# Optimization experiments

Measured on AMD Instinct MI355X. Metric: run time of the kernel, lower is better.

## Reference

```python
import jax, jax.numpy as jnp
import numpy as np

NUM_CLASSES = 80
STRIDES = (8, 16, 32)


def _decode(p, stride):
    # p: [B, 5+C, H, W] raw head -> [B, HW, 5+C] decoded (xy in px, wh=exp*stride)
    B, C, H, W = p.shape
    ys, xs = jnp.meshgrid(jnp.arange(H), jnp.arange(W), indexing='ij')
    grid = jnp.stack([xs, ys], -1).reshape(H * W, 2).astype(p.dtype)
    out = p.reshape(B, C, H * W).transpose(0, 2, 1)
    xy = (out[..., :2] + grid) * stride
    wh = jnp.exp(out[..., 2:4]) * stride
    out = jnp.concatenate([xy, wh, out[..., 4:]], -1)
    es = jnp.full((H * W,), float(stride), p.dtype)
    return out, grid[:, 0], grid[:, 1], es


def _pairwise_iou(gt, pr):
    # gt [G,4] cxcywh, pr [A,4] -> [G,A]
    gt_tl = gt[:, None, :2] - gt[:, None, 2:] * 0.5
    gt_br = gt[:, None, :2] + gt[:, None, 2:] * 0.5
    pr_tl = pr[None, :, :2] - pr[None, :, 2:] * 0.5
    pr_br = pr[None, :, :2] + pr[None, :, 2:] * 0.5
    tl = jnp.maximum(gt_tl, pr_tl)
    br = jnp.minimum(gt_br, pr_br)
    en = jnp.all(tl < br, -1).astype(gt.dtype)
    inter = jnp.prod(br - tl, -1) * en
    a_gt = jnp.prod(gt[:, 2:], -1)[:, None]
    a_pr = jnp.prod(pr[:, 2:], -1)[None, :]
    return inter / (a_gt + a_pr - inter + 1e-16)


def _assign(gt_boxes, gt_cls, bbox, clsp, objp, xg, yg, es):
    # SimOTA assignment for one image (all fixed-shape; non-candidate anchors
    # are masked out via huge cost instead of boolean gather).
    G = gt_boxes.shape[0]
    xc = (xg + 0.5) * es  # [A] anchor centers
    yc = (yg + 0.5) * es
    gl = gt_boxes[:, 0:1] - 0.5 * gt_boxes[:, 2:3]
    gr = gt_boxes[:, 0:1] + 0.5 * gt_boxes[:, 2:3]
    gt_ = gt_boxes[:, 1:2] - 0.5 * gt_boxes[:, 3:4]
    gb = gt_boxes[:, 1:2] + 0.5 * gt_boxes[:, 3:4]
    in_box = (xc[None] > gl) & (xc[None] < gr) & (yc[None] > gt_) & (yc[None] < gb)  # [G,A]
    r = 2.5 * es[None]
    in_ctr = ((xc[None] > gt_boxes[:, 0:1] - r) & (xc[None] < gt_boxes[:, 0:1] + r)
              & (yc[None] > gt_boxes[:, 1:2] - r) & (yc[None] < gt_boxes[:, 1:2] + r))
    fg_cand = jnp.any(in_box, 0) | jnp.any(in_ctr, 0)  # [A]
    in_both = in_box & in_ctr  # [G,A]

    ious = _pairwise_iou(gt_boxes, bbox)  # [G,A]
    ious_m = jnp.where(fg_cand[None, :], ious, 0.0)
    iou_cost = -jnp.log(ious_m + 1e-8)

    # pairwise cls BCE cost: bce(sqrt(sigmoid(cls)*sigmoid(obj)), onehot(gt)).sum(-1)
    p = jnp.sqrt(jax.nn.sigmoid(clsp) * jax.nn.sigmoid(objp[:, None]))  # [A,C]
    lp = jnp.maximum(jnp.log(p), -100.0)
    l1p = jnp.maximum(jnp.log1p(-p), -100.0)
    t = jax.nn.one_hot(gt_cls, NUM_CLASSES, dtype=p.dtype)  # [G,C]
    cls_cost = -(jnp.einsum('ac,gc->ga', lp - l1p, t) + jnp.sum(l1p, -1)[None, :])

    cost = (cls_cost + 3.0 * iou_cost
            + 1e5 * (~in_both).astype(p.dtype)
            + 1e9 * (~fg_cand)[None, :].astype(p.dtype))

    # dynamic-k: k_g = clamp(sum(top10 ious), min=1)
    topk_ious, _ = jax.lax.top_k(ious_m, 10)
    dyn_k = jnp.clip(topk_ious.sum(-1).astype(jnp.int32), 1, None)  # [G]
    rank = jnp.argsort(jnp.argsort(cost, axis=1), axis=1)  # rank of each anchor per gt
    matching = (rank < dyn_k[:, None]) & fg_cand[None, :]  # [G,A]
    # resolve anchors matched to multiple gts: keep min-cost gt
    multi = matching.sum(0) > 1
    best = jnp.argmin(cost, 0)
    matching = jnp.where(multi[None, :], jnp.arange(G)[:, None] == best[None, :], matching)

    fg = jnp.any(matching, 0)  # [A]
    matched_gt = jnp.argmax(matching, 0)  # [A]
    pred_iou = jnp.sum(matching * ious, 0)  # [A]
    matched_cls = gt_cls[matched_gt]
    return fg, matched_gt, pred_iou, matched_cls


def _giou_loss(b, g):
    tl = jnp.maximum(b[..., :2] - b[..., 2:] * 0.5, g[..., :2] - g[..., 2:] * 0.5)
    br = jnp.minimum(b[..., :2] + b[..., 2:] * 0.5, g[..., :2] + g[..., 2:] * 0.5)
    area_b = jnp.prod(b[..., 2:], -1)
    area_g = jnp.prod(g[..., 2:], -1)
    en = jnp.all(tl < br, -1).astype(b.dtype)
    inter = jnp.prod(br - tl, -1) * en
    union = area_b + area_g - inter
    iou = inter / (union + 1e-16)
    ctl = jnp.minimum(b[..., :2] - b[..., 2:] * 0.5, g[..., :2] - g[..., 2:] * 0.5)
    cbr = jnp.maximum(b[..., :2] + b[..., 2:] * 0.5, g[..., :2] + g[..., 2:] * 0.5)
    area_c = jnp.maximum(jnp.prod(cbr - ctl, -1), 1e-16)
    giou = iou - (area_c - union) / area_c
    return 1.0 - jnp.clip(giou, -1.0, 1.0)


def _bce_logits(x, t):
    return jnp.maximum(x, 0.0) - x * t + jnp.log1p(jnp.exp(-jnp.abs(x)))


def _forward(p8, p16, p32, labels):
    outs, xo, yo, eo = [], [], [], []
    for p, s in zip((p8, p16, p32), STRIDES):
        o, x, y, e = _decode(p, s)
        outs.append(o); xo.append(x); yo.append(y); eo.append(e)
    outputs = jnp.concatenate(outs, 1)  # [B, A, 5+C]
    xg = jnp.concatenate(xo); yg = jnp.concatenate(yo); es = jnp.concatenate(eo)

    bbox = outputs[..., :4]
    obj = outputs[..., 4]
    cls = outputs[..., 5:]
    gt_boxes = labels[..., :4]
    gt_cls = labels[..., 4].astype(jnp.int32)

    # assignment runs under no_grad in torch
    det = jax.lax.stop_gradient(outputs)
    fg, matched_gt, pred_iou, matched_cls = jax.vmap(
        lambda gb, gc, o: _assign(gb, gc, o[..., :4], o[..., 5:], o[..., 4], xg, yg, es)
    )(gt_boxes, gt_cls, det)

    fgf = fg.astype(outputs.dtype)  # [B,A]
    reg_t = jnp.take_along_axis(gt_boxes, matched_gt[..., None], axis=1)  # [B,A,4]
    cls_t = (jax.nn.one_hot(matched_cls, NUM_CLASSES, dtype=outputs.dtype)
             * pred_iou[..., None] * fgf[..., None])

    loss_iou = jnp.sum(_giou_loss(bbox, reg_t) * fgf)
    loss_obj = jnp.sum(_bce_logits(obj, fgf))
    loss_cls = jnp.sum(_bce_logits(cls, cls_t) * fgf[..., None])
    num_fg = jnp.maximum(jnp.sum(fgf), 1.0)
    return (5.0 * loss_iou + loss_obj + loss_cls) / num_fg


def setup_inputs() -> dict:
    key = jax.random.key(0)
    k1, k2, k3, k4, k5, k6 = jax.random.split(key, 6)
    B, NGT = 32, 20
    p8 = jax.random.normal(k1, (B, 5 + NUM_CLASSES, 80, 80), dtype=jnp.float32)
    p16 = jax.random.normal(k2, (B, 5 + NUM_CLASSES, 40, 40), dtype=jnp.float32)
    p32 = jax.random.normal(k3, (B, 5 + NUM_CLASSES, 20, 20), dtype=jnp.float32)
    cxy = jax.random.uniform(k4, (B, NGT, 2), dtype=jnp.float32, minval=32.0, maxval=608.0)
    wh = jax.random.uniform(k5, (B, NGT, 2), dtype=jnp.float32, minval=16.0, maxval=128.0)
    cls = jax.random.randint(k6, (B, NGT, 1), 0, NUM_CLASSES).astype(jnp.float32)
    labels = jnp.concatenate([cxy, wh, cls], -1)
    return {"p8": p8, "p16": p16, "p32": p32, "labels": labels}


def reference(p8, p16, p32, labels):
    return _forward(p8, p16, p32, labels)
```

## Files before the change

kernel.cpp:

```cpp
#include <hip/hip_runtime.h>
#include <cstdint>
#include <cstddef>

#define NA 8400
#define NAP 8448
#define NB 32
#define NG 20
#define NCL 80
#define NBLK 33
#define KC_BLKS 12

__device__ __forceinline__ float frcp(float x) { return __builtin_amdgcn_rcpf(x); }
__device__ __forceinline__ float bce0(float x) {
  return fmaxf(x, 0.0f) + __logf(1.0f + __expf(-fabsf(x)));
}

__device__ __forceinline__ void anchor_info(int a, const float* p8, const float* p16,
                                            const float* p32, int b, const float*& base,
                                            int& hw, int& HW, int& xg, int& yg, float& fs) {
  if (a < 6400)      { hw = a;        HW = 6400; xg = hw % 80; yg = hw / 80; fs = 8.f;
                       base = p8  + (size_t)b * 85 * 6400; }
  else if (a < 8000) { hw = a - 6400; HW = 1600; xg = hw % 40; yg = hw / 40; fs = 16.f;
                       base = p16 + (size_t)b * 85 * 1600; }
  else               { hw = a - 8000; HW = 400;  xg = hw % 20; yg = hw / 20; fs = 32.f;
                       base = p32 + (size_t)b * 85 * 400; }
}

__device__ __forceinline__ float iou_raw(float gx, float gy, float gw, float gh, float4 p) {
  float gtlx = gx - gw * 0.5f, gtly = gy - gh * 0.5f;
  float gbrx = gx + gw * 0.5f, gbry = gy + gh * 0.5f;
  float ptlx = p.x - p.z * 0.5f, ptly = p.y - p.w * 0.5f;
  float pbrx = p.x + p.z * 0.5f, pbry = p.y + p.w * 0.5f;
  float tlx = fmaxf(gtlx, ptlx), tly = fmaxf(gtly, ptly);
  float brx = fminf(gbrx, pbrx), bry = fminf(gbry, pbry);
  float inter = ((tlx < brx) && (tly < bry)) ? (brx - tlx) * (bry - tly) : 0.0f;
  float ag = gw * gh, ap = p.z * p.w;
  return inter * frcp(ag + ap - inter + 1e-16f);
}

__device__ __forceinline__ float giou_loss(float4 bb, float gx, float gy, float gw, float gh) {
  float btlx = bb.x - bb.z * 0.5f, btly = bb.y - bb.w * 0.5f;
  float bbrx = bb.x + bb.z * 0.5f, bbry = bb.y + bb.w * 0.5f;
  float gtlx = gx - gw * 0.5f, gtly = gy - gh * 0.5f;
  float gbrx = gx + gw * 0.5f, gbry = gy + gh * 0.5f;
  float tlx = fmaxf(btlx, gtlx), tly = fmaxf(btly, gtly);
  float brx = fminf(bbrx, gbrx), bry = fminf(bbry, gbry);
  float area_b = bb.z * bb.w, area_g = gw * gh;
  float inter = ((tlx < brx) && (tly < bry)) ? (brx - tlx) * (bry - tly) : 0.0f;
  float uni = area_b + area_g - inter;
  float iou = inter / (uni + 1e-16f);
  float ctlx = fminf(btlx, gtlx), ctly = fminf(btly, gtly);
  float cbrx = fmaxf(bbrx, gbrx), cbry = fmaxf(bbry, gbry);
  float area_c = fmaxf((cbrx - ctlx) * (cbry - ctly), 1e-16f);
  float giou = iou - (area_c - uni) / area_c;
  giou = fminf(fmaxf(giou, -1.0f), 1.0f);
  return 1.0f - giou;
}

__device__ __forceinline__ void block_argmin(float& v, int& i, volatile float* s_v,
                                             volatile int* s_i, int tid) {
#pragma unroll
  for (int off = 32; off; off >>= 1) {
    float ov = __shfl_down(v, off, 64);
    int   oi = __shfl_down(i, off, 64);
    if (ov < v || (ov == v && oi < i)) { v = ov; i = oi; }
  }
  if ((tid & 63) == 0) { s_v[tid >> 6] = v; s_i[tid >> 6] = i; }
  __syncthreads();
  v = s_v[0]; i = s_i[0];
#pragma unroll
  for (int w = 1; w < 4; ++w) {
    float ov = s_v[w]; int oi = s_i[w];
    if (ov < v || (ov == v && oi < i)) { v = ov; i = oi; }
  }
}

__global__ __launch_bounds__(256) void k1(const float* __restrict__ p8,
                                          const float* __restrict__ p16,
                                          const float* __restrict__ p32,
                                          const float* __restrict__ labels,
                                          int* __restrict__ n_fg_cnt,
                                          int* __restrict__ fg_list,
                                          unsigned int* __restrict__ am_c,
                                          float4* __restrict__ bbox_c,
                                          float* __restrict__ lso_c,
                                          unsigned int* __restrict__ match_c,
                                          float* __restrict__ blk_obj) {
  __shared__ float s_gt[NG * 4];
  __shared__ unsigned int s_wcnt[4];
  __shared__ float s_part[4];
  __shared__ unsigned int s_base;
  int blk = blockIdx.x, b = blockIdx.y, tid = threadIdx.x, lane = tid & 63, wid = tid >> 6;

  if (tid < NG) {
    s_gt[tid * 4 + 0] = labels[((size_t)b * NG + tid) * 5 + 0];
    s_gt[tid * 4 + 1] = labels[((size_t)b * NG + tid) * 5 + 1];
    s_gt[tid * 4 + 2] = labels[((size_t)b * NG + tid) * 5 + 2];
    s_gt[tid * 4 + 3] = labels[((size_t)b * NG + tid) * 5 + 3];
  }
  __syncthreads();

  int a = blk * 256 + tid;
  match_c[(size_t)b * NAP + a] = 0u;

  bool fg = false;
  unsigned int msk = 0u;
  float bce_obj = 0.0f, obj = 0.0f;
  const float* base = nullptr; int hw = 0, HW = 0, xg = 0, yg = 0; float fs = 8.f;
  if (a < NA) {
    anchor_info(a, p8, p16, p32, b, base, hw, HW, xg, yg, fs);
    obj = base[4 * HW + hw];
    bce_obj = bce0(obj);
    float xc = ((float)xg + 0.5f) * fs;
    float yc = ((float)yg + 0.5f) * fs;
    float r = 2.5f * fs;
#pragma unroll
    for (int g = 0; g < NG; ++g) {
      float gx = s_gt[g * 4 + 0], gy = s_gt[g * 4 + 1];
      float gw = s_gt[g * 4 + 2], gh = s_gt[g * 4 + 3];
      bool inb = (xc > gx - 0.5f * gw) && (xc < gx + 0.5f * gw) &&
                 (yc > gy - 0.5f * gh) && (yc < gy + 0.5f * gh);
      bool inc = (xc > gx - r) && (xc < gx + r) && (yc > gy - r) && (yc < gy + r);
      fg = fg || inb || inc;
      if (inb && inc) msk |= (1u << g);
    }
  }

  unsigned long long bm = __ballot(fg);
#pragma unroll
  for (int off = 32; off; off >>= 1) bce_obj += __shfl_down(bce_obj, off, 64);
  if (lane == 0) { s_wcnt[wid] = (unsigned int)__popcll(bm); s_part[wid] = bce_obj; }
  __syncthreads();
  if (tid == 0) {
    unsigned int cnt = s_wcnt[0] + s_wcnt[1] + s_wcnt[2] + s_wcnt[3];
    s_base = cnt ? (unsigned int)atomicAdd(&n_fg_cnt[b], (int)cnt) : 0u;
    blk_obj[b * NBLK + blk] = s_part[0] + s_part[1] + s_part[2] + s_part[3];
  }
  __syncthreads();

  if (!fg) return;
  unsigned int pos = s_base;
  for (int w = 0; w < wid; ++w) pos += s_wcnt[w];
  pos += (unsigned int)__popcll(bm & ((1ull << lane) - 1ull));
  size_t bo = (size_t)b * NAP;
  int ci = (int)pos;
  fg_list[bo + ci] = a;
  am_c[bo + ci] = msk;

  float v0 = base[hw];
  float v1 = base[HW + hw];
  float v2 = base[2 * HW + hw];
  float v3 = base[3 * HW + hw];
  bbox_c[bo + ci] = make_float4((v0 + (float)xg) * fs, (v1 + (float)yg) * fs,
                                __expf(v2) * fs, __expf(v3) * fs);
  float uo = __logf(1.0f + __expf(-fabsf(obj)));
  lso_c[bo + ci] = fminf(obj, 0.0f) - uo;
}

__global__ __launch_bounds__(256) void k2(const float* __restrict__ p8,
                                          const float* __restrict__ p16,
                                          const float* __restrict__ p32,
                                          const int* __restrict__ fg_list,
                                          const int* __restrict__ n_fg,
                                          const float* __restrict__ lso_c,
                                          float* __restrict__ sl_c,
                                          float* __restrict__ sb_c) {
  __shared__ float s_sl[8][33];
  __shared__ float s_sb[8][33];
  int b = blockIdx.y, tid = threadIdx.x;
  int part = tid >> 5, cl = tid & 31;
  int n = n_fg[b];
  size_t bo = (size_t)b * NAP;

  for (int base_ci = blockIdx.x * 32; base_ci < n; base_ci += gridDim.x * 32) {
    int ci = base_ci + cl;
    bool act = ci < n;
    float sl = 0.0f, sb = 0.0f;
    if (act) {
      int a = fg_list[bo + ci];
      float lso = lso_c[bo + ci];
      const float* base; int hw, HW, xg, yg; float fs;
      anchor_info(a, p8, p16, p32, b, base, hw, HW, xg, yg, fs);
      const float* cb = base + (size_t)(5 + part * 10) * HW + hw;
      float xs[10];
#pragma unroll
      for (int j = 0; j < 5; ++j) xs[j] = cb[j * HW];
#pragma unroll
      for (int j = 5; j < 10; ++j) xs[j] = cb[j * HW];
#pragma unroll
      for (int j = 0; j < 10; ++j) {
        float x = xs[j];
        float u = __logf(1.0f + __expf(-fabsf(x)));
        sb += fmaxf(x, 0.0f) + u;
        float lsx = fminf(x, 0.0f) - u;
        float lpr = 0.5f * (lsx + lso);
        float p   = __expf(lpr);
        sl += fmaxf(__logf(1.0f - p), -100.0f);
      }
    }
    s_sl[part][cl] = sl;
    s_sb[part][cl] = sb;
    __syncthreads();
    if (tid < 32 && base_ci + tid < n) {
      float tsl = 0.0f, tsb = 0.0f;
#pragma unroll
      for (int q = 0; q < 8; ++q) { tsl += s_sl[q][tid]; tsb += s_sb[q][tid]; }
      sl_c[bo + base_ci + tid] = tsl;
      sb_c[bo + base_ci + tid] = tsb;
    }
    __syncthreads();
  }
}

__global__ __launch_bounds__(256) void k3(const float* __restrict__ p8,
                                          const float* __restrict__ p16,
                                          const float* __restrict__ p32,
                                          const float* __restrict__ labels,
                                          const int* __restrict__ fg_list,
                                          const int* __restrict__ n_fg,
                                          const float* __restrict__ lso_c,
                                          const float* __restrict__ sl_c,
                                          const float4* __restrict__ bbox_c,
                                          const unsigned int* __restrict__ am_c,
                                          float* __restrict__ cost_tbl,
                                          float* __restrict__ iou_tbl) {
  int g = blockIdx.y, b = blockIdx.z, tid = threadIdx.x;
  int n = n_fg[b];
  size_t bo = (size_t)b * NAP;
  float gx = labels[((size_t)b * NG + g) * 5 + 0];
  float gy = labels[((size_t)b * NG + g) * 5 + 1];
  float gw = labels[((size_t)b * NG + g) * 5 + 2];
  float gh = labels[((size_t)b * NG + g) * 5 + 3];
  int   cg = (int)labels[((size_t)b * NG + g) * 5 + 4];
  size_t row = ((size_t)b * NG + g) * NAP;

  for (int ci = blockIdx.x * 256 + tid; ci < n; ci += gridDim.x * 256) {
    int a = fg_list[bo + ci];
    unsigned int am = am_c[bo + ci];
    float lso = lso_c[bo + ci];
    float sl  = sl_c[bo + ci];
    float4 pb = bbox_c[bo + ci];
    const float* base; int hw, HW, xg, yg; float fs;
    anchor_info(a, p8, p16, p32, b, base, hw, HW, xg, yg, fs);
    float x = base[(size_t)(5 + cg) * HW + hw];

    float u = __logf(1.0f + __expf(-fabsf(x)));
    float lsx = fminf(x, 0.0f) - u;
    float lpr = 0.5f * (lsx + lso);
    float p   = __expf(lpr);
    float l1p = fmaxf(__logf(1.0f - p), -100.0f);
    float wv  = fmaxf(lpr, -100.0f) - l1p;
    float iou = iou_raw(gx, gy, gw, gh, pb);
    float cst = -(wv + sl) - 3.0f * __logf(iou + 1e-8f);
    if (!((am >> g) & 1u)) cst += 100000.0f;
    cost_tbl[row + ci] = cst;
    iou_tbl[row + ci]  = iou;
  }
}

__global__ __launch_bounds__(256) void kB(const float* __restrict__ cost_tbl,
                                          const float* __restrict__ iou_tbl,
                                          const int* __restrict__ n_fg,
                                          unsigned int* __restrict__ match_c) {
  __shared__ float s_cost[NAP];
  __shared__ float s_wt[4 * 10];
  __shared__ float s_v[4];
  __shared__ int   s_i[4];
  __shared__ int   s_k;

  int g = blockIdx.x, b = blockIdx.y, tid = threadIdx.x;
  int lane = tid & 63, wid = tid >> 6;
  int n = n_fg[b];
  size_t bo = (size_t)b * NAP;
  const float* __restrict__ cg = cost_tbl + ((size_t)b * NG + g) * NAP;
  const float* __restrict__ ig = iou_tbl  + ((size_t)b * NG + g) * NAP;

  float t10[10];
#pragma unroll
  for (int j = 0; j < 10; ++j) t10[j] = 0.0f;

  for (int ci = tid; ci < n; ci += 256) {
    float iou = ig[ci];
    float cst = cg[ci];
    if (iou > t10[9]) {
      t10[9] = iou;
#pragma unroll
      for (int q = 9; q > 0; --q) {
        if (t10[q] > t10[q - 1]) { float t = t10[q]; t10[q] = t10[q - 1]; t10[q - 1] = t; }
        else break;
      }
    }
    s_cost[ci] = cst;
  }

  for (int r = 0; r < 10; ++r) {
    float v = t10[0];
    float bv = v;
#pragma unroll
    for (int off = 32; off; off >>= 1) bv = fmaxf(bv, __shfl_down(bv, off, 64));
    bv = __shfl(bv, 0, 64);
    unsigned long long won = __ballot(v == bv);
    if (lane == __ffsll(won) - 1) {
#pragma unroll
      for (int q = 0; q < 9; ++q) t10[q] = t10[q + 1];
      t10[9] = -1.0f;
    }
    if (lane == 0) s_wt[wid * 10 + r] = bv;
  }
  __syncthreads();

  if (tid == 0) {
    int p0 = 0, p1 = 0, p2 = 0, p3 = 0;
    float s = 0.0f;
    for (int r = 0; r < 10; ++r) {
      float v0 = (p0 < 10) ? s_wt[p0]      : -2.0f;
      float v1 = (p1 < 10) ? s_wt[10 + p1] : -2.0f;
      float v2 = (p2 < 10) ? s_wt[20 + p2] : -2.0f;
      float v3 = (p3 < 10) ? s_wt[30 + p3] : -2.0f;
      float m = fmaxf(fmaxf(v0, v1), fmaxf(v2, v3));
      s += m;
      if (m == v0) ++p0; else if (m == v1) ++p1; else if (m == v2) ++p2; else ++p3;
    }
    int k = (int)s;
    if (k < 1) k = 1;
    s_k = k;
  }
  __syncthreads();
  int k = s_k;

  for (int it = 0; it < k; ++it) {
    float bv = 3.4e38f; int bi = NAP;
    for (int ci = tid; ci < n; ci += 256) {
      float v = s_cost[ci];
      if (v < bv || (v == bv && ci < bi)) { bv = v; bi = ci; }
    }
    block_argmin(bv, bi, s_v, s_i, tid);
    if (bv >= 1e8f) break;
    if (tid == 0) {
      atomicOr(&match_c[bo + bi], 1u << g);
      s_cost[bi] = 3.4e38f;
    }
    __syncthreads();
  }
}

__global__ __launch_bounds__(256) void kCD(const float* __restrict__ p8,
                                           const float* __restrict__ p16,
                                           const float* __restrict__ p32,
                                           const float* __restrict__ labels,
                                           const float4* __restrict__ bbox_c,
                                           const float* __restrict__ sb_c,
                                           const float* __restrict__ cost_tbl,
                                           const float* __restrict__ iou_tbl,
                                           const int* __restrict__ fg_list,
                                           const int* __restrict__ n_fg,
                                           const unsigned int* __restrict__ match_c,
                                           const float* __restrict__ blk_obj,
                                           float* __restrict__ accum,
                                           int* __restrict__ done_cnt,
                                           float* __restrict__ out) {
  __shared__ float s_gt[NG * 5];
  __shared__ float s_red[16];
  __shared__ int s_last;
  int b = blockIdx.y, tid = threadIdx.x;
  if (tid < NG * 5) s_gt[tid] = labels[(size_t)b * NG * 5 + tid];
  __syncthreads();

  int n = n_fg[b];
  size_t bo = (size_t)b * NAP;
  float li = 0.0f, oe = 0.0f, lc = 0.0f, nf = 0.0f;

  for (int ci = blockIdx.x * 256 + tid; ci < n; ci += KC_BLKS * 256) {
    unsigned int m = match_c[bo + ci];
    if (m == 0u) continue;
    int mg;
    if (m & (m - 1)) {
      float bestc = 3.4e38f; mg = 0;
#pragma unroll 4
      for (int g = 0; g < NG; ++g) {
        float cst = cost_tbl[((size_t)b * NG + g) * NAP + ci];
        if (cst < bestc) { bestc = cst; mg = g; }
      }
    } else {
      mg = __ffs(m) - 1;
    }
    int a = fg_list[bo + ci];
    const float* base; int hw, HW, xg, yg; float fs;
    anchor_info(a, p8, p16, p32, b, base, hw, HW, xg, yg, fs);
    float4 pb = bbox_c[bo + ci];
    float gx = s_gt[mg * 5], gy = s_gt[mg * 5 + 1];
    float gw = s_gt[mg * 5 + 2], gh = s_gt[mg * 5 + 3];
    int cg = (int)s_gt[mg * 5 + 4];
    float piou = iou_tbl[((size_t)b * NG + mg) * NAP + ci];
    li += giou_loss(pb, gx, gy, gw, gh);
    float xcls = base[(size_t)(5 + cg) * HW + hw];
    lc += sb_c[bo + ci] - xcls * piou;
    oe += base[4 * HW + hw];
    nf += 1.0f;
  }

  float vals[4] = {li, oe, lc, nf};
#pragma unroll
  for (int q = 0; q < 4; ++q) {
#pragma unroll
    for (int off = 32; off; off >>= 1) vals[q] += __shfl_down(vals[q], off, 64);
  }
  if ((tid & 63) == 0) {
    int wid = tid >> 6;
    s_red[wid * 4 + 0] = vals[0];
    s_red[wid * 4 + 1] = vals[1];
    s_red[wid * 4 + 2] = vals[2];
    s_red[wid * 4 + 3] = vals[3];
  }
  __syncthreads();
  if (tid < 4) {
    const int slot[4] = {0, 2, 3, 4};
    float s = s_red[tid] + s_red[4 + tid] + s_red[8 + tid] + s_red[12 + tid];
    atomicAdd(&accum[slot[tid]], s);
  }

  if (tid == 0) {
    __threadfence();
    int old = atomicAdd(done_cnt, 1);
    s_last = (old == KC_BLKS * NB - 1) ? 1 : 0;
  }
  __syncthreads();
  if (s_last) {
    float s = 0.0f;
    for (int i = tid; i < NB * NBLK; i += 256) s += blk_obj[i];
#pragma unroll
    for (int off = 32; off; off >>= 1) s += __shfl_down(s, off, 64);
    if ((tid & 63) == 0) s_red[tid >> 6] = s;
    __syncthreads();
    if (tid == 0) {
      float obj_base = s_red[0] + s_red[1] + s_red[2] + s_red[3];
      float loss_iou = atomicAdd(&accum[0], 0.0f);
      float oex      = atomicAdd(&accum[2], 0.0f);
      float loss_cls = atomicAdd(&accum[3], 0.0f);
      float num_fg   = atomicAdd(&accum[4], 0.0f);
      float loss_obj = obj_base - oex;
      out[0] = (5.0f * loss_iou + loss_obj + loss_cls) / fmaxf(num_fg, 1.0f);
    }
  }
}

extern "C" void kernel_launch(void* const* d_in, const int* in_sizes, int n_in,
                              void* d_out, int out_size, void* d_ws, size_t ws_size,
                              hipStream_t stream) {
  const float* p8     = (const float*)d_in[0];
  const float* p16    = (const float*)d_in[1];
  const float* p32    = (const float*)d_in[2];
  const float* labels = (const float*)d_in[3];
  float* out = (float*)d_out;

  const size_t BAP = (size_t)NB * NAP;
  char* w = (char*)d_ws;
  float4*       bbox_c   = (float4*)w;
  float*        cost_tbl = (float*)(w + BAP * 16);
  float*        iou_tbl  = cost_tbl + (size_t)NB * NG * NAP;
  char*         w2       = (char*)(iou_tbl + (size_t)NB * NG * NAP);
  int*          fg_list  = (int*)(w2);
  unsigned int* match_c  = (unsigned int*)(w2 + BAP * 4);
  float*        sb_c     = (float*)(w2 + BAP * 8);
  float*        sl_c     = (float*)(w2 + BAP * 12);
  float*        lso_c    = (float*)(w2 + BAP * 16);
  unsigned int* am_c     = (unsigned int*)(w2 + BAP * 20);
  char*         w3       = w2 + BAP * 24;
  int*          n_fg     = (int*)w3;
  float*        accum    = (float*)(w3 + 128);
  int*          done_cnt = (int*)(w3 + 160);
  float*        blk_obj  = (float*)(w3 + 256);

  hipMemsetAsync(w3, 0, 256, stream);

  k1<<<dim3(NBLK, NB), dim3(256), 0, stream>>>(p8, p16, p32, labels, n_fg, fg_list, am_c,
                                               bbox_c, lso_c, match_c, blk_obj);
  k2<<<dim3(24, NB), dim3(256), 0, stream>>>(p8, p16, p32, fg_list, n_fg, lso_c, sl_c, sb_c);
  k3<<<dim3(12, NG, NB), dim3(256), 0, stream>>>(p8, p16, p32, labels, fg_list, n_fg, lso_c,
                                                 sl_c, bbox_c, am_c, cost_tbl, iou_tbl);
  kB<<<dim3(NG, NB), dim3(256), 0, stream>>>(cost_tbl, iou_tbl, n_fg, match_c);
  kCD<<<dim3(KC_BLKS, NB), dim3(256), 0, stream>>>(p8, p16, p32, labels, bbox_c, sb_c,
                                                   cost_tbl, iou_tbl, fg_list, n_fg,
                                                   match_c, blk_obj, accum, done_cnt, out);
}
```

Before: 173.4 us.

## Fuse cls-cost and per-GT cost kernels, and fold loss reduction into matching kernel

Merges the per-anchor class-sum kernel with the per-GT cost/IoU table kernel, so the summed log term stays in shared memory instead of a global sl_c buffer and the anchor metadata is loaded once per anchor. Also merges the top-k matching kernel with the final loss kernel: the last GT block per image, found with an atomic counter, computes that image's loss terms, and the last image finalizes the output. This removes two launches and one intermediate buffer. In exchange, the final per-image loss runs in a single block and the cost kernel uses fewer blocks.

```diff
diff --git a/kernel.cpp b/kernel.cpp
--- a/kernel.cpp
+++ b/kernel.cpp
@@ -8,7 +8,6 @@
 #define NG 20
 #define NCL 80
 #define NBLK 33
-#define KC_BLKS 12
 
 __device__ __forceinline__ float frcp(float x) { return __builtin_amdgcn_rcpf(x); }
 __device__ __forceinline__ float bce0(float x) {
@@ -157,36 +156,51 @@
   lso_c[bo + ci] = fminf(obj, 0.0f) - uo;
 }
 
-__global__ __launch_bounds__(256) void k2(const float* __restrict__ p8,
-                                          const float* __restrict__ p16,
-                                          const float* __restrict__ p32,
-                                          const int* __restrict__ fg_list,
-                                          const int* __restrict__ n_fg,
-                                          const float* __restrict__ lso_c,
-                                          float* __restrict__ sl_c,
-                                          float* __restrict__ sb_c) {
+__global__ __launch_bounds__(256) void k23(const float* __restrict__ p8,
+                                           const float* __restrict__ p16,
+                                           const float* __restrict__ p32,
+                                           const float* __restrict__ labels,
+                                           const int* __restrict__ fg_list,
+                                           const int* __restrict__ n_fg,
+                                           const float* __restrict__ lso_c,
+                                           const unsigned int* __restrict__ am_c,
+                                           const float4* __restrict__ bbox_c,
+                                           float* __restrict__ sb_c,
+                                           float* __restrict__ cost_tbl,
+                                           float* __restrict__ iou_tbl) {
+  __shared__ float s_gt[NG * 4];
+  __shared__ int   s_gcls[NG];
   __shared__ float s_sl[8][33];
   __shared__ float s_sb[8][33];
+  __shared__ float s_slr[32];
   int b = blockIdx.y, tid = threadIdx.x;
   int part = tid >> 5, cl = tid & 31;
+
+  if (tid < NG) {
+    s_gt[tid * 4 + 0] = labels[((size_t)b * NG + tid) * 5 + 0];
+    s_gt[tid * 4 + 1] = labels[((size_t)b * NG + tid) * 5 + 1];
+    s_gt[tid * 4 + 2] = labels[((size_t)b * NG + tid) * 5 + 2];
+    s_gt[tid * 4 + 3] = labels[((size_t)b * NG + tid) * 5 + 3];
+    s_gcls[tid] = (int)labels[((size_t)b * NG + tid) * 5 + 4];
+  }
+  __syncthreads();
+
   int n = n_fg[b];
   size_t bo = (size_t)b * NAP;
 
   for (int base_ci = blockIdx.x * 32; base_ci < n; base_ci += gridDim.x * 32) {
     int ci = base_ci + cl;
     bool act = ci < n;
-    float sl = 0.0f, sb = 0.0f;
+    const float* base = nullptr; int hw = 0, HW = 0, xg, yg; float fs;
+    float lso = 0.0f, sl = 0.0f, sb = 0.0f;
     if (act) {
       int a = fg_list[bo + ci];
-      float lso = lso_c[bo + ci];
-      const float* base; int hw, HW, xg, yg; float fs;
+      lso = lso_c[bo + ci];
       anchor_info(a, p8, p16, p32, b, base, hw, HW, xg, yg, fs);
       const float* cb = base + (size_t)(5 + part * 10) * HW + hw;
       float xs[10];
 #pragma unroll
-      for (int j = 0; j < 5; ++j) xs[j] = cb[j * HW];
-#pragma unroll
-      for (int j = 5; j < 10; ++j) xs[j] = cb[j * HW];
+      for (int j = 0; j < 10; ++j) xs[j] = cb[(size_t)j * HW];
 #pragma unroll
       for (int j = 0; j < 10; ++j) {
         float x = xs[j];
@@ -201,72 +215,68 @@
     s_sl[part][cl] = sl;
     s_sb[part][cl] = sb;
     __syncthreads();
-    if (tid < 32 && base_ci + tid < n) {
+    if (tid < 32) {
       float tsl = 0.0f, tsb = 0.0f;
 #pragma unroll
       for (int q = 0; q < 8; ++q) { tsl += s_sl[q][tid]; tsb += s_sb[q][tid]; }
-      sl_c[bo + base_ci + tid] = tsl;
-      sb_c[bo + base_ci + tid] = tsb;
+      s_slr[tid] = tsl;
+      if (base_ci + tid < n) sb_c[bo + base_ci + tid] = tsb;
     }
     __syncthreads();
-  }
-}
-
-__global__ __launch_bounds__(256) void k3(const float* __restrict__ p8,
-                                          const float* __restrict__ p16,
-                                          const float* __restrict__ p32,
-                                          const float* __restrict__ labels,
-                                          const int* __restrict__ fg_list,
-                                          const int* __restrict__ n_fg,
-                                          const float* __restrict__ lso_c,
-                                          const float* __restrict__ sl_c,
-                                          const float4* __restrict__ bbox_c,
-                                          const unsigned int* __restrict__ am_c,
-                                          float* __restrict__ cost_tbl,
-                                          float* __restrict__ iou_tbl) {
-  int g = blockIdx.y, b = blockIdx.z, tid = threadIdx.x;
-  int n = n_fg[b];
-  size_t bo = (size_t)b * NAP;
-  float gx = labels[((size_t)b * NG + g) * 5 + 0];
-  float gy = labels[((size_t)b * NG + g) * 5 + 1];
-  float gw = labels[((size_t)b * NG + g) * 5 + 2];
-  float gh = labels[((size_t)b * NG + g) * 5 + 3];
-  int   cg = (int)labels[((size_t)b * NG + g) * 5 + 4];
-  size_t row = ((size_t)b * NG + g) * NAP;
-
-  for (int ci = blockIdx.x * 256 + tid; ci < n; ci += gridDim.x * 256) {
-    int a = fg_list[bo + ci];
-    unsigned int am = am_c[bo + ci];
-    float lso = lso_c[bo + ci];
-    float sl  = sl_c[bo + ci];
-    float4 pb = bbox_c[bo + ci];
-    const float* base; int hw, HW, xg, yg; float fs;
-    anchor_info(a, p8, p16, p32, b, base, hw, HW, xg, yg, fs);
-    float x = base[(size_t)(5 + cg) * HW + hw];
-
-    float u = __logf(1.0f + __expf(-fabsf(x)));
-    float lsx = fminf(x, 0.0f) - u;
-    float lpr = 0.5f * (lsx + lso);
-    float p   = __expf(lpr);
-    float l1p = fmaxf(__logf(1.0f - p), -100.0f);
-    float wv  = fmaxf(lpr, -100.0f) - l1p;
-    float iou = iou_raw(gx, gy, gw, gh, pb);
-    float cst = -(wv + sl) - 3.0f * __logf(iou + 1e-8f);
-    if (!((am >> g) & 1u)) cst += 100000.0f;
-    cost_tbl[row + ci] = cst;
-    iou_tbl[row + ci]  = iou;
-  }
-}
-
-__global__ __launch_bounds__(256) void kB(const float* __restrict__ cost_tbl,
-                                          const float* __restrict__ iou_tbl,
-                                          const int* __restrict__ n_fg,
-                                          unsigned int* __restrict__ match_c) {
+    if (act) {
+      float slr = s_slr[cl];
+      unsigned int am = am_c[bo + ci];
+      float4 pb = bbox_c[bo + ci];
+#pragma unroll
+      for (int gg = 0; gg < 3; ++gg) {
+        int g = part + (gg << 3);
+        if (g < NG) {
+          int cg = s_gcls[g];
+          float x = base[(size_t)(5 + cg) * HW + hw];
+          float u = __logf(1.0f + __expf(-fabsf(x)));
+          float lsx = fminf(x, 0.0f) - u;
+          float lpr = 0.5f * (lsx + lso);
+          float p   = __expf(lpr);
+          float l1p = fmaxf(__logf(1.0f - p), -100.0f);
+          float wv  = fmaxf(lpr, -100.0f) - l1p;
+          float iou = iou_raw(s_gt[g * 4 + 0], s_gt[g * 4 + 1],
+                              s_gt[g * 4 + 2], s_gt[g * 4 + 3], pb);
+          float cst = -(wv + slr) - 3.0f * __logf(iou + 1e-8f);
+          if (!((am >> g) & 1u)) cst += 100000.0f;
+          size_t row = ((size_t)b * NG + g) * NAP;
+          cost_tbl[row + ci] = cst;
+          iou_tbl[row + ci]  = iou;
+        }
+      }
+    }
+    __syncthreads();
+  }
+}
+
+__global__ __launch_bounds__(256) void kBCD(const float* __restrict__ p8,
+                                            const float* __restrict__ p16,
+                                            const float* __restrict__ p32,
+                                            const float* __restrict__ labels,
+                                            const float* __restrict__ cost_tbl,
+                                            const float* __restrict__ iou_tbl,
+                                            const int* __restrict__ n_fg,
+                                            unsigned int* __restrict__ match_c,
+                                            const int* __restrict__ fg_list,
+                                            const float4* __restrict__ bbox_c,
+                                            const float* __restrict__ sb_c,
+                                            const float* __restrict__ blk_obj,
+                                            float* __restrict__ accum,
+                                            int* __restrict__ done_g,
+                                            int* __restrict__ done_img,
+                                            float* __restrict__ out) {
   __shared__ float s_cost[NAP];
   __shared__ float s_wt[4 * 10];
   __shared__ float s_v[4];
   __shared__ int   s_i[4];
   __shared__ int   s_k;
+  __shared__ int   s_flag;
+  __shared__ float s_gt[NG * 5];
+  __shared__ float s_red[16];
 
   int g = blockIdx.x, b = blockIdx.y, tid = threadIdx.x;
   int lane = tid & 63, wid = tid >> 6;
@@ -342,44 +352,29 @@
     }
     __syncthreads();
   }
-}
-
-__global__ __launch_bounds__(256) void kCD(const float* __restrict__ p8,
-                                           const float* __restrict__ p16,
-                                           const float* __restrict__ p32,
-                                           const float* __restrict__ labels,
-                                           const float4* __restrict__ bbox_c,
-                                           const float* __restrict__ sb_c,
-                                           const float* __restrict__ cost_tbl,
-                                           const float* __restrict__ iou_tbl,
-                                           const int* __restrict__ fg_list,
-                                           const int* __restrict__ n_fg,
-                                           const unsigned int* __restrict__ match_c,
-                                           const float* __restrict__ blk_obj,
-                                           float* __restrict__ accum,
-                                           int* __restrict__ done_cnt,
-                                           float* __restrict__ out) {
-  __shared__ float s_gt[NG * 5];
-  __shared__ float s_red[16];
-  __shared__ int s_last;
-  int b = blockIdx.y, tid = threadIdx.x;
+
+  __syncthreads();
+  if (tid == 0) {
+    __threadfence();
+    s_flag = (atomicAdd(&done_g[b], 1) == NG - 1) ? 1 : 0;
+  }
+  __syncthreads();
+  if (!s_flag) return;
+
   if (tid < NG * 5) s_gt[tid] = labels[(size_t)b * NG * 5 + tid];
   __syncthreads();
 
-  int n = n_fg[b];
-  size_t bo = (size_t)b * NAP;
   float li = 0.0f, oe = 0.0f, lc = 0.0f, nf = 0.0f;
-
-  for (int ci = blockIdx.x * 256 + tid; ci < n; ci += KC_BLKS * 256) {
-    unsigned int m = match_c[bo + ci];
+  for (int ci = tid; ci < n; ci += 256) {
+    unsigned int m = atomicOr(&match_c[bo + ci], 0u);
     if (m == 0u) continue;
     int mg;
     if (m & (m - 1)) {
       float bestc = 3.4e38f; mg = 0;
 #pragma unroll 4
-      for (int g = 0; g < NG; ++g) {
-        float cst = cost_tbl[((size_t)b * NG + g) * NAP + ci];
-        if (cst < bestc) { bestc = cst; mg = g; }
+      for (int gq = 0; gq < NG; ++gq) {
+        float cst = cost_tbl[((size_t)b * NG + gq) * NAP + ci];
+        if (cst < bestc) { bestc = cst; mg = gq; }
       }
     } else {
       mg = __ffs(m) - 1;
@@ -390,10 +385,10 @@
     float4 pb = bbox_c[bo + ci];
     float gx = s_gt[mg * 5], gy = s_gt[mg * 5 + 1];
     float gw = s_gt[mg * 5 + 2], gh = s_gt[mg * 5 + 3];
-    int cg = (int)s_gt[mg * 5 + 4];
+    int cgq = (int)s_gt[mg * 5 + 4];
     float piou = iou_tbl[((size_t)b * NG + mg) * NAP + ci];
     li += giou_loss(pb, gx, gy, gw, gh);
-    float xcls = base[(size_t)(5 + cg) * HW + hw];
+    float xcls = base[(size_t)(5 + cgq) * HW + hw];
     lc += sb_c[bo + ci] - xcls * piou;
     oe += base[4 * HW + hw];
     nf += 1.0f;
@@ -406,11 +401,11 @@
     for (int off = 32; off; off >>= 1) vals[q] += __shfl_down(vals[q], off, 64);
   }
   if ((tid & 63) == 0) {
-    int wid = tid >> 6;
-    s_red[wid * 4 + 0] = vals[0];
-    s_red[wid * 4 + 1] = vals[1];
-    s_red[wid * 4 + 2] = vals[2];
-    s_red[wid * 4 + 3] = vals[3];
+    int w = tid >> 6;
+    s_red[w * 4 + 0] = vals[0];
+    s_red[w * 4 + 1] = vals[1];
+    s_red[w * 4 + 2] = vals[2];
+    s_red[w * 4 + 3] = vals[3];
   }
   __syncthreads();
   if (tid < 4) {
@@ -421,26 +416,25 @@
 
   if (tid == 0) {
     __threadfence();
-    int old = atomicAdd(done_cnt, 1);
-    s_last = (old == KC_BLKS * NB - 1) ? 1 : 0;
-  }
-  __syncthreads();
-  if (s_last) {
-    float s = 0.0f;
-    for (int i = tid; i < NB * NBLK; i += 256) s += blk_obj[i];
-#pragma unroll
-    for (int off = 32; off; off >>= 1) s += __shfl_down(s, off, 64);
-    if ((tid & 63) == 0) s_red[tid >> 6] = s;
-    __syncthreads();
-    if (tid == 0) {
-      float obj_base = s_red[0] + s_red[1] + s_red[2] + s_red[3];
-      float loss_iou = atomicAdd(&accum[0], 0.0f);
-      float oex      = atomicAdd(&accum[2], 0.0f);
-      float loss_cls = atomicAdd(&accum[3], 0.0f);
-      float num_fg   = atomicAdd(&accum[4], 0.0f);
-      float loss_obj = obj_base - oex;
-      out[0] = (5.0f * loss_iou + loss_obj + loss_cls) / fmaxf(num_fg, 1.0f);
-    }
+    s_flag = (atomicAdd(done_img, 1) == NB - 1) ? 1 : 0;
+  }
+  __syncthreads();
+  if (!s_flag) return;
+
+  float s = 0.0f;
+  for (int i = tid; i < NB * NBLK; i += 256) s += blk_obj[i];
+#pragma unroll
+  for (int off = 32; off; off >>= 1) s += __shfl_down(s, off, 64);
+  if ((tid & 63) == 0) s_red[tid >> 6] = s;
+  __syncthreads();
+  if (tid == 0) {
+    float obj_base = s_red[0] + s_red[1] + s_red[2] + s_red[3];
+    float loss_iou = atomicAdd(&accum[0], 0.0f);
+    float oex      = atomicAdd(&accum[2], 0.0f);
+    float loss_cls = atomicAdd(&accum[3], 0.0f);
+    float num_fg   = atomicAdd(&accum[4], 0.0f);
+    float loss_obj = obj_base - oex;
+    out[0] = (5.0f * loss_iou + loss_obj + loss_cls) / fmaxf(num_fg, 1.0f);
   }
 }
 
@@ -462,24 +456,22 @@
   int*          fg_list  = (int*)(w2);
   unsigned int* match_c  = (unsigned int*)(w2 + BAP * 4);
   float*        sb_c     = (float*)(w2 + BAP * 8);
-  float*        sl_c     = (float*)(w2 + BAP * 12);
-  float*        lso_c    = (float*)(w2 + BAP * 16);
-  unsigned int* am_c     = (unsigned int*)(w2 + BAP * 20);
-  char*         w3       = w2 + BAP * 24;
+  float*        lso_c    = (float*)(w2 + BAP * 12);
+  unsigned int* am_c     = (unsigned int*)(w2 + BAP * 16);
+  char*         w3       = w2 + BAP * 20;
   int*          n_fg     = (int*)w3;
   float*        accum    = (float*)(w3 + 128);
-  int*          done_cnt = (int*)(w3 + 160);
-  float*        blk_obj  = (float*)(w3 + 256);
-
-  hipMemsetAsync(w3, 0, 256, stream);
+  int*          done_g   = (int*)(w3 + 256);
+  int*          done_img = (int*)(w3 + 384);
+  float*        blk_obj  = (float*)(w3 + 512);
+
+  hipMemsetAsync(w3, 0, 512, stream);
 
   k1<<<dim3(NBLK, NB), dim3(256), 0, stream>>>(p8, p16, p32, labels, n_fg, fg_list, am_c,
                                                bbox_c, lso_c, match_c, blk_obj);
-  k2<<<dim3(24, NB), dim3(256), 0, stream>>>(p8, p16, p32, fg_list, n_fg, lso_c, sl_c, sb_c);
-  k3<<<dim3(12, NG, NB), dim3(256), 0, stream>>>(p8, p16, p32, labels, fg_list, n_fg, lso_c,
-                                                 sl_c, bbox_c, am_c, cost_tbl, iou_tbl);
-  kB<<<dim3(NG, NB), dim3(256), 0, stream>>>(cost_tbl, iou_tbl, n_fg, match_c);
-  kCD<<<dim3(KC_BLKS, NB), dim3(256), 0, stream>>>(p8, p16, p32, labels, bbox_c, sb_c,
-                                                   cost_tbl, iou_tbl, fg_list, n_fg,
-                                                   match_c, blk_obj, accum, done_cnt, out);
-}
+  k23<<<dim3(NBLK, NB), dim3(256), 0, stream>>>(p8, p16, p32, labels, fg_list, n_fg, lso_c,
+                                                am_c, bbox_c, sb_c, cost_tbl, iou_tbl);
+  kBCD<<<dim3(NG, NB), dim3(256), 0, stream>>>(p8, p16, p32, labels, cost_tbl, iou_tbl,
+                                               n_fg, match_c, fg_list, bbox_c, sb_c,
+                                               blk_obj, accum, done_g, done_img, out);
+}
```

Result: no change. 173.2 us (-0.1%).
